# Kernel optimization log

Hardware: AMD Instinct MI355X
Metric: run time of the kernel (lower is better)

The kernel has to match this reference:

```python
import jax, jax.numpy as jnp
import numpy as np
import math

B, T, INP_DIM, OUT_DIM = 2, 4096, 1, 64
DEPTH, D_MODEL, N_HEADS, D_FF = 4, 512, 8, 2048
D_HEAD = D_MODEL // N_HEADS
EPS = 1e-5


def setup_inputs() -> dict:
    key = jax.random.key(0)
    ks = jax.random.split(key, 16)
    s = 0.02
    inp = {
        "x_in": jax.random.normal(ks[0], (B, T, INP_DIM), dtype=jnp.float32),
        "inp_w": jax.random.normal(ks[1], (INP_DIM, D_MODEL), dtype=jnp.float32) * s,
        "inp_b": jnp.zeros((D_MODEL,), dtype=jnp.float32),
        "pos_emb": jax.random.normal(ks[2], (T, D_MODEL), dtype=jnp.float32) * s,
        "ln1_g": jnp.ones((DEPTH, D_MODEL), dtype=jnp.float32),
        "ln1_b": jnp.zeros((DEPTH, D_MODEL), dtype=jnp.float32),
        "qkv_w": jax.random.normal(ks[3], (DEPTH, D_MODEL, 3 * D_MODEL), dtype=jnp.float32) * s,
        "proj_w": jax.random.normal(ks[4], (DEPTH, D_MODEL, D_MODEL), dtype=jnp.float32) * s,
        "ln2_g": jnp.ones((DEPTH, D_MODEL), dtype=jnp.float32),
        "ln2_b": jnp.zeros((DEPTH, D_MODEL), dtype=jnp.float32),
        "fc1_w": jax.random.normal(ks[5], (DEPTH, D_MODEL, D_FF), dtype=jnp.float32) * s,
        "fc2_w": jax.random.normal(ks[6], (DEPTH, D_FF, D_MODEL), dtype=jnp.float32) * s,
        "lnf_g": jnp.ones((D_MODEL,), dtype=jnp.float32),
        "lnf_b": jnp.zeros((D_MODEL,), dtype=jnp.float32),
        "head_w": jax.random.normal(ks[7], (D_MODEL, OUT_DIM), dtype=jnp.float32) * s,
        "head_b": jnp.zeros((OUT_DIM,), dtype=jnp.float32),
    }
    return inp


def _layernorm(x, g, b):
    mu = jnp.mean(x, axis=-1, keepdims=True)
    var = jnp.mean(jnp.square(x - mu), axis=-1, keepdims=True)
    return (x - mu) * jax.lax.rsqrt(var + EPS) * g + b


def _attn(x, qkv_w, proj_w):
    Bx, Tx, d = x.shape
    qkv = x @ qkv_w  # [B,T,3d]
    q, k, v = jnp.split(qkv, 3, axis=-1)
    q = q.reshape(Bx, Tx, N_HEADS, D_HEAD)
    k = k.reshape(Bx, Tx, N_HEADS, D_HEAD)
    v = v.reshape(Bx, Tx, N_HEADS, D_HEAD)
    scores = jnp.einsum('bqhd,bkhd->bhqk', q, k) / math.sqrt(D_HEAD)
    causal = jnp.tril(jnp.ones((Tx, Tx), dtype=bool))
    scores = jnp.where(causal, scores, -jnp.inf)
    attn = jax.nn.softmax(scores, axis=-1)
    out = jnp.einsum('bhqk,bkhd->bqhd', attn, v).reshape(Bx, Tx, d)
    return out @ proj_w


def reference(x_in, inp_w, inp_b, pos_emb, ln1_g, ln1_b, qkv_w, proj_w,
              ln2_g, ln2_b, fc1_w, fc2_w, lnf_g, lnf_b, head_w, head_b):
    x = x_in @ inp_w + inp_b + pos_emb[None, :, :]  # [B,T,d]
    for l in range(DEPTH):
        x = x + _attn(_layernorm(x, ln1_g[l], ln1_b[l]), qkv_w[l], proj_w[l])
        h = _layernorm(x, ln2_g[l], ln2_b[l])
        h = jax.nn.gelu(h @ fc1_w[l], approximate=False) @ fc2_w[l]
        x = x + h
    h = _layernorm(x, lnf_g, lnf_b)
    return h @ head_w + head_b  # [B,T,out_dim]
```

## Files before the change

kernel.cpp:

```cpp
#include <hip/hip_runtime.h>
#include <math.h>

typedef unsigned short u16;
typedef unsigned int u32;

#define B_ 2
#define T_ 4096
#define DM 512
#define NH 8
#define DH 64
#define DFF 2048
#define MTOT (B_*T_)

#define SCALEQ 0.18033688011112042f

using f32x4  = __attribute__((ext_vector_type(4))) float;
using f32x16 = __attribute__((ext_vector_type(16))) float;
using bf16x8 = __attribute__((ext_vector_type(8))) short;
typedef unsigned int u32x2 __attribute__((ext_vector_type(2)));

__device__ __forceinline__ float b2f(u16 u) {
  union { u32 u; float f; } v; v.u = ((u32)u) << 16; return v.f;
}
__device__ __forceinline__ u16 f2b(float f) {
  union { float f; u32 u; } v; v.f = f;
  u32 r = v.u + 0x7FFFu + ((v.u >> 16) & 1u);
  return (u16)(r >> 16);
}
__device__ __forceinline__ u32 cvtpk(float lo, float hi) {
  u32 r;
  asm("v_cvt_pk_bf16_f32 %0, %1, %2" : "=v"(r) : "v"(lo), "v"(hi));
  return r;
}
#if __has_builtin(__builtin_amdgcn_exp2f)
#define EXP2(x) __builtin_amdgcn_exp2f(x)
#else
#define EXP2(x) __expf((x) * 0.6931471805599453f)
#endif
#if __has_builtin(__builtin_amdgcn_rcpf)
#define RCP(x) __builtin_amdgcn_rcpf(x)
#else
#define RCP(x) (1.0f / (x))
#endif

__device__ __forceinline__ void gload_lds(const u16* g, u16* l) {
  __builtin_amdgcn_global_load_lds(
      (const __attribute__((address_space(1))) void*)g,
      (__attribute__((address_space(3))) void*)l, 16, 0, 0);
}

__device__ __forceinline__ int lsw(int row, int col) {
  int slot = ((col >> 3) + (row >> 3) + 2 * (row & 7)) & 7;
  return (row << 6) + (slot << 3) + (col & 7);
}

__global__ __launch_bounds__(256) void embed_k(
    const float* __restrict__ x_in, const float* __restrict__ w,
    const float* __restrict__ bias, const float* __restrict__ pos,
    float* __restrict__ x) {
  int idx = blockIdx.x * 256 + threadIdx.x;
  int row = idx >> 9, d = idx & 511;
  int t = row & (T_ - 1);
  x[idx] = x_in[row] * w[d] + bias[d] + pos[t * DM + d];
}

template<int NP>
__global__ __launch_bounds__(256) void ln_k(
    float* __restrict__ x, const u16* __restrict__ P,
    const float* __restrict__ g, const float* __restrict__ bet,
    u16* __restrict__ y) {
  int wid = threadIdx.x >> 6, lane = threadIdx.x & 63;
  int row = blockIdx.x * 4 + wid;
  float* xr = x + (size_t)row * DM + lane * 8;
  float4 a0 = *(const float4*)xr;
  float4 a1 = *(const float4*)(xr + 4);
  float v[8] = {a0.x, a0.y, a0.z, a0.w, a1.x, a1.y, a1.z, a1.w};
  if (NP > 0) {
#pragma unroll
    for (int s = 0; s < NP; s++) {
      const u16* pr = P + (size_t)s * MTOT * DM + (size_t)row * DM + lane * 8;
      uint4 pv = *(const uint4*)pr;
      const u16* px = (const u16*)&pv;
#pragma unroll
      for (int j = 0; j < 8; j++) v[j] += b2f(px[j]);
    }
    float4 w0; w0.x = v[0]; w0.y = v[1]; w0.z = v[2]; w0.w = v[3];
    float4 w1; w1.x = v[4]; w1.y = v[5]; w1.z = v[6]; w1.w = v[7];
    *(float4*)xr = w0;
    *(float4*)(xr + 4) = w1;
  }
  float s = 0.f;
#pragma unroll
  for (int j = 0; j < 8; j++) s += v[j];
#pragma unroll
  for (int off = 32; off; off >>= 1) s += __shfl_xor(s, off);
  float mu = s * (1.0f / DM);
  float q = 0.f;
#pragma unroll
  for (int j = 0; j < 8; j++) { float e = v[j] - mu; q += e * e; }
#pragma unroll
  for (int off = 32; off; off >>= 1) q += __shfl_xor(q, off);
  float rs = rsqrtf(q * (1.0f / DM) + 1e-5f);
  float4 g0 = *(const float4*)(g + lane * 8);
  float4 g1 = *(const float4*)(g + lane * 8 + 4);
  float4 p0 = *(const float4*)(bet + lane * 8);
  float4 p1 = *(const float4*)(bet + lane * 8 + 4);
  float gg[8] = {g0.x, g0.y, g0.z, g0.w, g1.x, g1.y, g1.z, g1.w};
  float pp[8] = {p0.x, p0.y, p0.z, p0.w, p1.x, p1.y, p1.z, p1.w};
  uint4 st;
  st.x = cvtpk((v[0]-mu)*rs*gg[0]+pp[0], (v[1]-mu)*rs*gg[1]+pp[1]);
  st.y = cvtpk((v[2]-mu)*rs*gg[2]+pp[2], (v[3]-mu)*rs*gg[3]+pp[3]);
  st.z = cvtpk((v[4]-mu)*rs*gg[4]+pp[4], (v[5]-mu)*rs*gg[5]+pp[5]);
  st.w = cvtpk((v[6]-mu)*rs*gg[6]+pp[6], (v[7]-mu)*rs*gg[7]+pp[7]);
  *(uint4*)(y + (size_t)row * DM + lane * 8) = st;
}

__global__ __launch_bounds__(256) void wconv_k(
    const float* __restrict__ W, u16* __restrict__ Wt, int K, int N) {
  __shared__ float tile[32][33];
  const float* Wl = W + (size_t)blockIdx.z * K * N;
  u16* Wtl = Wt + (size_t)blockIdx.z * K * N;
  int k0 = blockIdx.x * 32, n0 = blockIdx.y * 32;
  int r = threadIdx.x >> 3, c4 = (threadIdx.x & 7) * 4;
  *(float4*)&tile[r][c4] = *(const float4*)(Wl + (size_t)(k0 + r) * N + n0 + c4);
  __syncthreads();
  uint2 st;
  st.x = cvtpk(tile[c4 + 0][r], tile[c4 + 1][r]);
  st.y = cvtpk(tile[c4 + 2][r], tile[c4 + 3][r]);
  *(uint2*)(Wtl + (size_t)(n0 + r) * K + k0 + c4) = st;
}

template<int EPI>
__global__ __launch_bounds__(256) void gemm_k(
    const u16* __restrict__ A, const u16* __restrict__ Bt,
    u16* __restrict__ Cb, float* __restrict__ Cf,
    int M, int N, int K, int Kslice, int scale_cols) {
  __shared__ u16 As[2][128][32];
  __shared__ u16 Bs[2][128][32];
  int tid = threadIdx.x;
  int lane = tid & 63, wid = tid >> 6;
  int wr = wid >> 1, wc = wid & 1;
  int nwg = gridDim.x * gridDim.y;
  int flat = blockIdx.y * gridDim.x + blockIdx.x;
  int swz = (flat & 7) * (nwg >> 3) + (flat >> 3);
  int bx = swz % gridDim.x, by = swz / gridDim.x;
  int m0 = by * 128, n0 = bx * 128;
  int kbeg = blockIdx.z * Kslice;
  if (EPI == 4) Cb += (size_t)blockIdx.z * M * N;
  f32x4 acc[4][4] = {};
  int rsub = lane >> 2, ksub = (lane & 3) * 8;
  const u16* Ab = A  + (size_t)(m0 + wid * 32 + rsub) * K + kbeg + ksub;
  const u16* Bb = Bt + (size_t)(n0 + wid * 32 + rsub) * K + kbeg + ksub;
#define GSTAGE(BUF, KO) { \
    gload_lds(Ab + (KO), &As[BUF][wid * 32][0]); \
    gload_lds(Ab + (size_t)16 * K + (KO), &As[BUF][wid * 32 + 16][0]); \
    gload_lds(Bb + (KO), &Bs[BUF][wid * 32][0]); \
    gload_lds(Bb + (size_t)16 * K + (KO), &Bs[BUF][wid * 32 + 16][0]); }
  GSTAGE(0, 0);
  __syncthreads();
  int r = lane & 15, kc = (lane >> 4) * 8;
  for (int k0 = 0; k0 < Kslice; k0 += 32) {
    int cur = (k0 >> 5) & 1;
    if (k0 + 32 < Kslice) GSTAGE(cur ^ 1, k0 + 32);
    bf16x8 af[4], bfr[4];
#pragma unroll
    for (int m = 0; m < 4; m++) af[m]  = *(const bf16x8*)&As[cur][wr*64 + m*16 + r][kc];
#pragma unroll
    for (int n = 0; n < 4; n++) bfr[n] = *(const bf16x8*)&Bs[cur][wc*64 + n*16 + r][kc];
#pragma unroll
    for (int m = 0; m < 4; m++)
#pragma unroll
      for (int n = 0; n < 4; n++)
        acc[m][n] = __builtin_amdgcn_mfma_f32_16x16x32_bf16(af[m], bfr[n], acc[m][n], 0, 0, 0);
    __syncthreads();
  }
  int r4 = (lane >> 4) * 4, cN = lane & 15;
#pragma unroll
  for (int m = 0; m < 4; m++) {
#pragma unroll
    for (int n = 0; n < 4; n++) {
      int col = n0 + wc*64 + n*16 + cN;
#pragma unroll
      for (int i = 0; i < 4; i++) {
        int row = m0 + wr*64 + m*16 + r4 + i;
        size_t off = (size_t)row * N + col;
        float v = acc[m][n][i];
        if (EPI == 0) {
          if (col < scale_cols) v *= SCALEQ;
          Cb[off] = f2b(v);
        } else if (EPI == 1) {
          Cf[off] += v;
        } else if (EPI == 4) {
          Cb[off] = f2b(v);
        } else {
          float e = EXP2(v * (2.3022082f + 0.10294324f * v * v));
          Cb[off] = f2b(v * (1.0f - RCP(e + 1.0f)));
        }
      }
    }
  }
}

#if __has_builtin(__builtin_amdgcn_permlane32_swap)
#define PLSWAP(A, B, O0, O1) { \
    u32x2 r_ = __builtin_amdgcn_permlane32_swap((A), (B), false, false); \
    O0 = r_.x; O1 = r_.y; }
#else
#define PLSWAP(A, B, O0, O1) { \
    u32 as_ = __shfl_xor((u32)(A), 32), bs_ = __shfl_xor((u32)(B), 32); \
    O0 = hh ? bs_ : (A); O1 = hh ? (B) : as_; }
#endif

__global__ __launch_bounds__(256) void attn_k(const u16* __restrict__ qkv,
                                              u16* __restrict__ Opart,
                                              float* __restrict__ ml) {
  __shared__ u16 Ks[2][64 * 64];
  __shared__ u16 Vt[2][64 * 64];
  int tid = threadIdx.x;
  int w = tid >> 6, l = tid & 63;
  int hh = l >> 5, c = l & 31;
  int flat = blockIdx.y * 144 + blockIdx.x;
  int swz = (flat & 7) * 288 + (flat >> 3);
  int bh = swz / 144, slot = swz - bh * 144;
  int g = 0;
  while (2 * (g + 1) * (g + 2) <= slot) g++;
  int s2 = slot - 2 * g * (g + 1);
  int qb = 4 * g + s2 / (g + 1);
  int ck = s2 - (s2 / (g + 1)) * (g + 1);
  int ntot = 2 * qb + 2;
  int kt0 = ck * 8;
  int kt1 = kt0 + 8 < ntot ? kt0 + 8 : ntot;
  int b = bh >> 3, hd = bh & 7;
  int q0w = qb * 128 + w * 32;
  int q_abs = q0w + c;
  size_t base = (size_t)b * T_ * 1536;
  bf16x8 qf[4];
  const u16* qp = qkv + base + (size_t)q_abs * 1536 + hd * 64 + hh * 8;
#pragma unroll
  for (int kk = 0; kk < 4; kk++) qf[kk] = *(const bf16x8*)(qp + kk * 16);
  f32x16 oa0 = {}, oa1 = {};
  float m_run = -1e30f, l_run = 0.f;
  int sp = tid >> 3, d8 = (tid & 7) * 8;
  int r0 = sp * 2, r1 = r0 + 1;
  const u16* kvbase = qkv + base + DM + hd * 64 + d8;
  uint4 kreg0, kreg1, vreg0, vreg1;
#define AGLOAD(KT) { \
    const u16* s0_ = kvbase + (size_t)((KT) * 64 + r0) * 1536; \
    kreg0 = *(const uint4*)s0_; vreg0 = *(const uint4*)(s0_ + DM); \
    const u16* s1_ = s0_ + 1536; \
    kreg1 = *(const uint4*)s1_; vreg1 = *(const uint4*)(s1_ + DM); }
  AGLOAD(kt0);
  for (int kt = kt0; kt < kt1; kt++) {
    u16* Kb = Ks[kt & 1];
    u16* Vb = Vt[kt & 1];
    *(uint4*)&Kb[lsw(r0, d8)] = kreg0;
    *(uint4*)&Kb[lsw(r1, d8)] = kreg1;
    {
      const u16* v0 = (const u16*)&vreg0;
      const u16* v1 = (const u16*)&vreg1;
#pragma unroll
      for (int j = 0; j < 8; j++) {
        u32 pw = (u32)v0[j] | ((u32)v1[j] << 16);
        *(u32*)&Vb[lsw(d8 + j, r0)] = pw;
      }
    }
    __syncthreads();
    if (kt + 1 < kt1) AGLOAD(kt + 1);
    if (kt * 64 > q0w + 31) continue;
    bool needMask = (kt * 64 + 63 > q0w);
    f32x16 sa0 = {}, sa1 = {};
    __builtin_amdgcn_s_setprio(1);
#pragma unroll
    for (int kk = 0; kk < 4; kk++) {
      bf16x8 ka  = *(const bf16x8*)&Kb[lsw(c,      kk * 16 + hh * 8)];
      bf16x8 kb2 = *(const bf16x8*)&Kb[lsw(32 + c, kk * 16 + hh * 8)];
      sa0 = __builtin_amdgcn_mfma_f32_32x32x16_bf16(ka,  qf[kk], sa0, 0, 0, 0);
      sa1 = __builtin_amdgcn_mfma_f32_32x32x16_bf16(kb2, qf[kk], sa1, 0, 0, 0);
    }
    __builtin_amdgcn_s_setprio(0);
    if (needMask) {
#pragma unroll
      for (int gi = 0; gi < 4; gi++)
#pragma unroll
        for (int i = 0; i < 4; i++) {
          int krow = kt * 64 + gi * 8 + hh * 4 + i;
          if (krow > q_abs)      sa0[gi * 4 + i] = -1e30f;
          if (krow + 32 > q_abs) sa1[gi * 4 + i] = -1e30f;
        }
    }
    float t[8];
#pragma unroll
    for (int r = 0; r < 8; r++)
      t[r] = fmaxf(fmaxf(sa0[r], sa0[r + 8]), fmaxf(sa1[r], sa1[r + 8]));
    float pm = fmaxf(fmaxf(fmaxf(t[0], t[1]), fmaxf(t[2], t[3])),
                     fmaxf(fmaxf(t[4], t[5]), fmaxf(t[6], t[7])));
    pm = fmaxf(pm, __shfl_xor(pm, 32));
    if (!__all(pm - m_run <= 8.0f)) {
      float mnew = fmaxf(m_run, pm);
      float corr = EXP2(m_run - mnew);
      l_run *= corr;
#pragma unroll
      for (int r = 0; r < 16; r++) { oa0[r] *= corr; oa1[r] *= corr; }
      m_run = mnew;
    }
    float sarr[16];
#pragma unroll
    for (int r = 0; r < 16; r++) {
      float e0 = EXP2(sa0[r] - m_run); sa0[r] = e0;
      float e1 = EXP2(sa1[r] - m_run); sa1[r] = e1;
      sarr[r] = e0 + e1;
    }
#pragma unroll
    for (int r = 0; r < 8; r++) sarr[r] += sarr[r + 8];
#pragma unroll
    for (int r = 0; r < 4; r++) sarr[r] += sarr[r + 4];
    float lsum = (sarr[0] + sarr[1]) + (sarr[2] + sarr[3]);
    lsum += __shfl_xor(lsum, 32);
    l_run += lsum;
    u32 Aw[8], Bw_[8];
#pragma unroll
    for (int r2 = 0; r2 < 4; r2++) {
      Aw[r2]      = cvtpk(sa0[4 * r2 + 0], sa0[4 * r2 + 1]);
      Bw_[r2]     = cvtpk(sa0[4 * r2 + 2], sa0[4 * r2 + 3]);
      Aw[4 + r2]  = cvtpk(sa1[4 * r2 + 0], sa1[4 * r2 + 1]);
      Bw_[4 + r2] = cvtpk(sa1[4 * r2 + 2], sa1[4 * r2 + 3]);
    }
    __builtin_amdgcn_s_setprio(1);
#pragma unroll
    for (int ks = 0; ks < 4; ks++) {
      int mo = (ks >> 1) * 4;
      int r2e = mo + 2 * (ks & 1), r2o = r2e + 1;
      union { u32 wd[4]; bf16x8 v; } u;
      PLSWAP(Aw[r2e], Aw[r2o], u.wd[0], u.wd[2]);
      PLSWAP(Bw_[r2e], Bw_[r2o], u.wd[1], u.wd[3]);
      bf16x8 va = *(const bf16x8*)&Vb[lsw(c,      ks * 16 + hh * 8)];
      bf16x8 vb = *(const bf16x8*)&Vb[lsw(32 + c, ks * 16 + hh * 8)];
      oa0 = __builtin_amdgcn_mfma_f32_32x32x16_bf16(va, u.v, oa0, 0, 0, 0);
      oa1 = __builtin_amdgcn_mfma_f32_32x32x16_bf16(vb, u.v, oa1, 0, 0, 0);
    }
    __builtin_amdgcn_s_setprio(0);
  }
  int sidx = bh * 144 + slot;
  u16* op = Opart + ((size_t)sidx * 128 + w * 32 + c) * 64;
#pragma unroll
  for (int gi = 0; gi < 4; gi++) {
    uint2 s0, s1;
    s0.x = cvtpk(oa0[4*gi+0], oa0[4*gi+1]);
    s0.y = cvtpk(oa0[4*gi+2], oa0[4*gi+3]);
    s1.x = cvtpk(oa1[4*gi+0], oa1[4*gi+1]);
    s1.y = cvtpk(oa1[4*gi+2], oa1[4*gi+3]);
    int d0 = gi * 8 + hh * 4;
    *(uint2*)(op + d0)      = s0;
    *(uint2*)(op + 32 + d0) = s1;
  }
  if (hh == 0) {
    float2 p; p.x = m_run; p.y = l_run;
    *(float2*)&ml[((size_t)sidx * 128 + w * 32 + c) * 2] = p;
  }
}

__global__ __launch_bounds__(256) void comb_k(
    const u16* __restrict__ Opart, const float* __restrict__ ml,
    u16* __restrict__ attno) {
  int gi = blockIdx.x * 256 + threadIdx.x;
  int d4 = (gi & 15) * 4;
  int bhq = gi >> 4;
  int bh = bhq >> 12, q = bhq & 4095;
  int qb = q >> 7, ri = q & 127;
  int g = qb >> 2;
  int nc = g + 1;
  int bs = 2 * g * (g + 1) + (qb & 3) * (g + 1);
  int s0 = bh * 144 + bs;
  float M = -1e30f;
  for (int cc = 0; cc < nc; cc++)
    M = fmaxf(M, ml[((size_t)(s0 + cc) * 128 + ri) * 2]);
  float O0 = 0.f, O1 = 0.f, O2 = 0.f, O3 = 0.f, L = 0.f;
  for (int cc = 0; cc < nc; cc++) {
    float2 p = *(const float2*)&ml[((size_t)(s0 + cc) * 128 + ri) * 2];
    float wgt = EXP2(p.x - M);
    L += p.y * wgt;
    uint2 ov = *(const uint2*)&Opart[((size_t)(s0 + cc) * 128 + ri) * 64 + d4];
    const u16* opx = (const u16*)&ov;
    O0 += b2f(opx[0]) * wgt; O1 += b2f(opx[1]) * wgt;
    O2 += b2f(opx[2]) * wgt; O3 += b2f(opx[3]) * wgt;
  }
  float invL = 1.0f / L;
  int b = bh >> 3, hd = bh & 7;
  uint2 st;
  st.x = cvtpk(O0 * invL, O1 * invL);
  st.y = cvtpk(O2 * invL, O3 * invL);
  *(uint2*)&attno[((size_t)b * T_ + q) * DM + hd * 64 + d4] = st;
}

__global__ __launch_bounds__(256) void head_k(
    const u16* __restrict__ xb, const float* __restrict__ W,
    const float* __restrict__ bias, float* __restrict__ out) {
  int wid = threadIdx.x >> 6, lane = threadIdx.x & 63;
  int row = blockIdx.x * 4 + wid;
  const u16* xr = xb + (size_t)row * DM;
  float a0 = 0.f, a1 = 0.f, a2 = 0.f, a3 = 0.f;
  for (int d = 0; d < DM; d += 8) {
    uint4 xv = *(const uint4*)(xr + d);
    const u16* xp = (const u16*)&xv;
    const float* Wp = W + (size_t)d * 64 + lane;
    a0 += b2f(xp[0]) * Wp[0];
    a1 += b2f(xp[1]) * Wp[64];
    a2 += b2f(xp[2]) * Wp[128];
    a3 += b2f(xp[3]) * Wp[192];
    a0 += b2f(xp[4]) * Wp[256];
    a1 += b2f(xp[5]) * Wp[320];
    a2 += b2f(xp[6]) * Wp[384];
    a3 += b2f(xp[7]) * Wp[448];
  }
  out[(size_t)row * 64 + lane] = a0 + a1 + a2 + a3 + bias[lane];
}

extern "C" void kernel_launch(void* const* d_in, const int* in_sizes, int n_in,
                              void* d_out, int out_size, void* d_ws, size_t ws_size,
                              hipStream_t stream) {
  (void)in_sizes; (void)n_in; (void)out_size; (void)ws_size;
  const float* x_in  = (const float*)d_in[0];
  const float* inp_w = (const float*)d_in[1];
  const float* inp_b = (const float*)d_in[2];
  const float* pos   = (const float*)d_in[3];
  const float* ln1g  = (const float*)d_in[4];
  const float* ln1b  = (const float*)d_in[5];
  const float* qkvw  = (const float*)d_in[6];
  const float* projw = (const float*)d_in[7];
  const float* ln2g  = (const float*)d_in[8];
  const float* ln2b  = (const float*)d_in[9];
  const float* fc1w  = (const float*)d_in[10];
  const float* fc2w  = (const float*)d_in[11];
  const float* lnfg  = (const float*)d_in[12];
  const float* lnfb  = (const float*)d_in[13];
  const float* headw = (const float*)d_in[14];
  const float* headb = (const float*)d_in[15];

  char* ws = (char*)d_ws;
  size_t off = 0;
  float* x     = (float*)(ws + off); off += (size_t)MTOT * DM * 4;
  u16*  lnb    = (u16*)(ws + off);   off += (size_t)MTOT * DM * 2;
  u16*  qkvb   = (u16*)(ws + off);   off += (size_t)MTOT * 3 * DM * 2;
  u16*  attno  = (u16*)(ws + off);   off += (size_t)MTOT * DM * 2;
  u16*  ff     = qkvb;
  u16*  qkvt   = (u16*)(ws + off);   off += (size_t)4 * DM * 3 * DM * 2;
  u16*  projt  = (u16*)(ws + off);   off += (size_t)4 * DM * DM * 2;
  u16*  fc1t   = (u16*)(ws + off);   off += (size_t)4 * DM * DFF * 2;
  u16*  fc2t   = (u16*)(ws + off);   off += (size_t)4 * DFF * DM * 2;
  char* shared = ws + off;
  u16*  Opart  = (u16*)shared;
  float* mlbuf = (float*)(shared + (size_t)16 * 144 * 128 * 64 * 2);
  u16*  fcp    = (u16*)shared;

  wconv_k<<<dim3(16, 48, 4), 256, 0, stream>>>(qkvw,  qkvt, DM, 3 * DM);
  wconv_k<<<dim3(16, 16, 4), 256, 0, stream>>>(projw, projt, DM, DM);
  wconv_k<<<dim3(16, 64, 4), 256, 0, stream>>>(fc1w,  fc1t, DM, DFF);
  wconv_k<<<dim3(64, 16, 4), 256, 0, stream>>>(fc2w,  fc2t, DFF, DM);

  embed_k<<<(MTOT * DM) / 256, 256, 0, stream>>>(x_in, inp_w, inp_b, pos, x);
  for (int ly = 0; ly < 4; ly++) {
    if (ly == 0)
      ln_k<0><<<MTOT / 4, 256, 0, stream>>>(x, nullptr, ln1g, ln1b, lnb);
    else
      ln_k<2><<<MTOT / 4, 256, 0, stream>>>(x, fcp, ln1g + ly * DM, ln1b + ly * DM, lnb);
    gemm_k<0><<<dim3(12, 64), 256, 0, stream>>>(lnb, qkvt + (size_t)ly * DM * 3 * DM,
                                                qkvb, nullptr, MTOT, 3 * DM, DM, DM, DM);
    attn_k<<<dim3(144, 16), 256, 0, stream>>>(qkvb, Opart, mlbuf);
    comb_k<<<(16 * 4096 * 16) / 256, 256, 0, stream>>>(Opart, mlbuf, attno);
    gemm_k<4><<<dim3(4, 64, 2), 256, 0, stream>>>(attno, projt + (size_t)ly * DM * DM,
                                                  fcp, nullptr, MTOT, DM, DM, DM / 2, 0);
    ln_k<2><<<MTOT / 4, 256, 0, stream>>>(x, fcp, ln2g + ly * DM, ln2b + ly * DM, lnb);
    gemm_k<2><<<dim3(16, 64), 256, 0, stream>>>(lnb, fc1t + (size_t)ly * DM * DFF,
                                                ff, nullptr, MTOT, DFF, DM, DM, 0);
    gemm_k<4><<<dim3(4, 64, 2), 256, 0, stream>>>(ff, fc2t + (size_t)ly * DFF * DM,
                                                  fcp, nullptr, MTOT, DM, DFF, DFF / 2, 0);
  }
  ln_k<2><<<MTOT / 4, 256, 0, stream>>>(x, fcp, lnfg, lnfb, lnb);
  head_k<<<MTOT / 4, 256, 0, stream>>>(lnb, headw, headb, (float*)d_out);
}
```

Before: 859.9 us.

## Load attention K tiles directly to LDS and raise split-K to four

In the attention kernel, K tiles now go from global memory straight into LDS through gload_lds with a pre-swizzled source address, so they no longer pass through registers. The V prefetch for the next tile is moved later, after the softmax, to overlap it with compute and lower register pressure. Separately, the projection and FC2 GEMMs move from 2-way to 4-way split-K, and the layernorm kernel now sums four partials. This adds parallelism for the N=512 GEMMs at the cost of more partial-sum traffic. It also depends on the ln_k<4> template and the workspace already supporting four partial buffers.

```diff
diff --git a/kernel.cpp b/kernel.cpp
--- a/kernel.cpp
+++ b/kernel.cpp
@@ -240,22 +240,31 @@
   for (int kk = 0; kk < 4; kk++) qf[kk] = *(const bf16x8*)(qp + kk * 16);
   f32x16 oa0 = {}, oa1 = {};
   float m_run = -1e30f, l_run = 0.f;
+  const u16* kvb = qkv + base + DM + hd * 64;
+  int lr = l >> 3, ls = l & 7;
+  int rA = w * 8 + lr;
+  int rB = (w + 4) * 8 + lr;
+  int cA = ((ls - w - 2 * (rA & 7)) & 7) * 8;
+  int cB = ((ls - (w + 4) - 2 * (rB & 7)) & 7) * 8;
+  const u16* ksrcA = kvb + (size_t)rA * 1536 + cA;
+  const u16* ksrcB = kvb + (size_t)rB * 1536 + cB;
   int sp = tid >> 3, d8 = (tid & 7) * 8;
-  int r0 = sp * 2, r1 = r0 + 1;
-  const u16* kvbase = qkv + base + DM + hd * 64 + d8;
-  uint4 kreg0, kreg1, vreg0, vreg1;
-#define AGLOAD(KT) { \
-    const u16* s0_ = kvbase + (size_t)((KT) * 64 + r0) * 1536; \
-    kreg0 = *(const uint4*)s0_; vreg0 = *(const uint4*)(s0_ + DM); \
-    const u16* s1_ = s0_ + 1536; \
-    kreg1 = *(const uint4*)s1_; vreg1 = *(const uint4*)(s1_ + DM); }
-  AGLOAD(kt0);
+  int r0 = sp * 2;
+  uint4 vreg0, vreg1;
+#define KGLOAD(KT) { \
+    size_t ko_ = (size_t)(KT) * 64 * 1536; int nx_ = (KT) & 1; \
+    gload_lds(ksrcA + ko_, &Ks[nx_][w * 512]); \
+    gload_lds(ksrcB + ko_, &Ks[nx_][(w + 4) * 512]); }
+#define AGV(KT) { \
+    const u16* s_ = kvb + DM + (size_t)((KT) * 64 + r0) * 1536 + d8; \
+    vreg0 = *(const uint4*)s_; vreg1 = *(const uint4*)(s_ + 1536); }
+  KGLOAD(kt0);
+  AGV(kt0);
   for (int kt = kt0; kt < kt1; kt++) {
-    u16* Kb = Ks[kt & 1];
-    u16* Vb = Vt[kt & 1];
-    *(uint4*)&Kb[lsw(r0, d8)] = kreg0;
-    *(uint4*)&Kb[lsw(r1, d8)] = kreg1;
+    int cur = kt & 1;
+    bool more = (kt + 1 < kt1);
     {
+      u16* Vb = Vt[cur];
       const u16* v0 = (const u16*)&vreg0;
       const u16* v1 = (const u16*)&vreg1;
 #pragma unroll
@@ -265,8 +274,13 @@
       }
     }
     __syncthreads();
-    if (kt + 1 < kt1) AGLOAD(kt + 1);
-    if (kt * 64 > q0w + 31) continue;
+    if (more) KGLOAD(kt + 1);
+    if (kt * 64 > q0w + 31) {
+      if (more) AGV(kt + 1);
+      continue;
+    }
+    const u16* Kb = Ks[cur];
+    const u16* Vb = Vt[cur];
     bool needMask = (kt * 64 + 63 > q0w);
     f32x16 sa0 = {}, sa1 = {};
     __builtin_amdgcn_s_setprio(1);
@@ -325,6 +339,7 @@
       Aw[4 + r2]  = cvtpk(sa1[4 * r2 + 0], sa1[4 * r2 + 1]);
       Bw_[4 + r2] = cvtpk(sa1[4 * r2 + 2], sa1[4 * r2 + 3]);
     }
+    if (more) AGV(kt + 1);
     __builtin_amdgcn_s_setprio(1);
 #pragma unroll
     for (int ks = 0; ks < 4; ks++) {
@@ -462,19 +477,19 @@
     if (ly == 0)
       ln_k<0><<<MTOT / 4, 256, 0, stream>>>(x, nullptr, ln1g, ln1b, lnb);
     else
-      ln_k<2><<<MTOT / 4, 256, 0, stream>>>(x, fcp, ln1g + ly * DM, ln1b + ly * DM, lnb);
+      ln_k<4><<<MTOT / 4, 256, 0, stream>>>(x, fcp, ln1g + ly * DM, ln1b + ly * DM, lnb);
     gemm_k<0><<<dim3(12, 64), 256, 0, stream>>>(lnb, qkvt + (size_t)ly * DM * 3 * DM,
                                                 qkvb, nullptr, MTOT, 3 * DM, DM, DM, DM);
     attn_k<<<dim3(144, 16), 256, 0, stream>>>(qkvb, Opart, mlbuf);
     comb_k<<<(16 * 4096 * 16) / 256, 256, 0, stream>>>(Opart, mlbuf, attno);
-    gemm_k<4><<<dim3(4, 64, 2), 256, 0, stream>>>(attno, projt + (size_t)ly * DM * DM,
-                                                  fcp, nullptr, MTOT, DM, DM, DM / 2, 0);
-    ln_k<2><<<MTOT / 4, 256, 0, stream>>>(x, fcp, ln2g + ly * DM, ln2b + ly * DM, lnb);
+    gemm_k<4><<<dim3(4, 64, 4), 256, 0, stream>>>(attno, projt + (size_t)ly * DM * DM,
+                                                  fcp, nullptr, MTOT, DM, DM, DM / 4, 0);
+    ln_k<4><<<MTOT / 4, 256, 0, stream>>>(x, fcp, ln2g + ly * DM, ln2b + ly * DM, lnb);
     gemm_k<2><<<dim3(16, 64), 256, 0, stream>>>(lnb, fc1t + (size_t)ly * DM * DFF,
                                                 ff, nullptr, MTOT, DFF, DM, DM, 0);
-    gemm_k<4><<<dim3(4, 64, 2), 256, 0, stream>>>(ff, fc2t + (size_t)ly * DFF * DM,
-                                                  fcp, nullptr, MTOT, DM, DFF, DFF / 2, 0);
-  }
-  ln_k<2><<<MTOT / 4, 256, 0, stream>>>(x, fcp, lnfg, lnfb, lnb);
+    gemm_k<4><<<dim3(4, 64, 4), 256, 0, stream>>>(ff, fc2t + (size_t)ly * DFF * DM,
+                                                  fcp, nullptr, MTOT, DM, DFF, DFF / 4, 0);
+  }
+  ln_k<4><<<MTOT / 4, 256, 0, stream>>>(x, fcp, lnfg, lnfb, lnb);
   head_k<<<MTOT / 4, 256, 0, stream>>>(lnb, headw, headb, (float*)d_out);
 }
```

New measurement: 928.9 us. 1.08x slower.
